# Optimization experiments

Hardware: AMD Instinct MI355X
Metric: run time of the kernel (lower is better)

## Reference

```python
import jax, jax.numpy as jnp
import numpy as np

EPS = 1e-5


def _bn(x, gamma, beta, mean, var):
    # Inference-mode BatchNorm2d over channel dim (NCHW -> axis 1).
    inv = gamma / jnp.sqrt(var + EPS)
    return x * inv[None, :, None, None] + (beta - mean * inv)[None, :, None, None]


def setup_inputs() -> dict:
    key = jax.random.key(0)
    ks = jax.random.split(key, 6)
    N, Cin, Cout, T, V = 64, 64, 128, 300, 25
    x = jax.random.normal(ks[0], (N, Cin, T, V), dtype=jnp.float32)
    A = jax.random.uniform(ks[1], (V, V), dtype=jnp.float32)  # fixed adjacency (non-trainable buffer)
    edge = jnp.ones((V, V), dtype=jnp.float32)                # learnable edge mask, init ones
    gcn_w = jax.random.normal(ks[2], (Cout, Cin), dtype=jnp.float32) * 0.05
    gcn_b = jnp.zeros((Cout,), dtype=jnp.float32)
    res_w = jax.random.normal(ks[3], (Cout, Cin), dtype=jnp.float32) * 0.05
    res_b = jnp.zeros((Cout,), dtype=jnp.float32)
    return {
        'x': x, 'A': A, 'edge': edge,
        'gcn_w': gcn_w, 'gcn_b': gcn_b,
        'bn_gamma': jnp.ones((Cout,), jnp.float32), 'bn_beta': jnp.zeros((Cout,), jnp.float32),
        'bn_mean': jnp.zeros((Cout,), jnp.float32), 'bn_var': jnp.ones((Cout,), jnp.float32),
        'res_w': res_w, 'res_b': res_b,
        'rbn_gamma': jnp.ones((Cout,), jnp.float32), 'rbn_beta': jnp.zeros((Cout,), jnp.float32),
        'rbn_mean': jnp.zeros((Cout,), jnp.float32), 'rbn_var': jnp.ones((Cout,), jnp.float32),
    }


def reference(x, A, edge, gcn_w, gcn_b, bn_gamma, bn_beta, bn_mean, bn_var,
              res_w, res_b, rbn_gamma, rbn_beta, rbn_mean, rbn_var):
    # x: [N, Cin, T, V]
    # residual branch: 1x1 conv + BN (in_channel != out_channel path)
    res = jnp.einsum('oc,nctv->notv', res_w, x) + res_b[None, :, None, None]
    res = _bn(res, rbn_gamma, rbn_beta, rbn_mean, rbn_var)
    # main branch: 1x1 conv -> adjacency einsum -> BN
    y = jnp.einsum('oc,nctv->notv', gcn_w, x) + gcn_b[None, :, None, None]
    y = jnp.einsum('nctv,vw->nctw', y, A * edge)
    y = _bn(y, bn_gamma, bn_beta, bn_mean, bn_var)
    # keep_prob = 1.0 -> Randomized_DropBlock_Ske / DropBlockT_1d are identity
    return jax.nn.relu(y + res)
```

## Files before the change

kernel.cpp:

```cpp
#include <hip/hip_runtime.h>
#include <stdint.h>

#define N_ 64
#define C_ 64
#define O_ 128
#define T_ 300
#define V_ 25
#define TB 4
#define JB (TB * 32)
#define KB 128
#define LDB 136

typedef __attribute__((ext_vector_type(8))) short short8;
typedef __attribute__((ext_vector_type(4))) float floatx4;

__device__ __forceinline__ short f2bf(float f) {
  unsigned u = __float_as_uint(f);
  unsigned r = (u + 0x7FFFu + ((u >> 16) & 1u)) >> 16;
  return (short)(r & 0xFFFFu);
}

__global__ void sgc_prep(const float* __restrict__ A, const float* __restrict__ edge,
                         const float* __restrict__ gcn_w, const float* __restrict__ gcn_b,
                         const float* __restrict__ bn_g, const float* __restrict__ bn_b,
                         const float* __restrict__ bn_m, const float* __restrict__ bn_v,
                         const float* __restrict__ res_w, const float* __restrict__ res_b,
                         const float* __restrict__ rg, const float* __restrict__ rb,
                         const float* __restrict__ rm, const float* __restrict__ rv,
                         short* __restrict__ Wcat, float* __restrict__ M2p,
                         float* __restrict__ Cwp) {
  const int tid = threadIdx.x;
  for (int i = tid; i < 25 * 32; i += 256) {
    const int v = i >> 5, w = i & 31;
    M2p[i] = (w < 25) ? A[v * 25 + w] * edge[v * 25 + w] : 0.f;
  }
  for (int i = tid; i < O_ * 32; i += 256) {
    const int o = i >> 5, w = i & 31;
    const float inv1 = bn_g[o] * rsqrtf(bn_v[o] + 1e-5f);
    const float inv2 = rg[o] * rsqrtf(rv[o] + 1e-5f);
    float S = 0.f;
    if (w < 25) {
      for (int v = 0; v < 25; ++v) S += A[v * 25 + w] * edge[v * 25 + w];
    }
    Cwp[i] = inv1 * gcn_b[o] * S + (bn_b[o] - bn_m[o] * inv1) + inv2 * res_b[o] +
             (rb[o] - rm[o] * inv2);
  }
  for (int i = tid; i < O_ * KB; i += 256) {
    const int o = i >> 7, k = i & 127;
    const float inv1 = bn_g[o] * rsqrtf(bn_v[o] + 1e-5f);
    const float inv2 = rg[o] * rsqrtf(rv[o] + 1e-5f);
    const float val = (k < 64) ? inv2 * res_w[o * 64 + k] : inv1 * gcn_w[o * 64 + (k - 64)];
    Wcat[i] = f2bf(val);
  }
}

__global__ __launch_bounds__(256, 2) void sgc_main(const float* __restrict__ x,
                                                   const short* __restrict__ Wcat,
                                                   const float* __restrict__ M2p,
                                                   const float* __restrict__ Cw,
                                                   float* __restrict__ out) {
  __shared__ short Bs[JB * LDB];
  const int tid = threadIdx.x;
  const int b = blockIdx.x;
  const int n = b / 75;
  const int t0 = (b % 75) * TB;

  {
    const int tl = tid >> 6;
    const int c = tid & 63;
    const float* xrow = x + (((n * C_ + c) * T_) + (t0 + tl)) * V_;
    float xr[25];
#pragma unroll
    for (int v = 0; v < 25; ++v) xr[v] = xrow[v];
#pragma unroll
    for (int v = 0; v < 25; ++v) Bs[(tl * 32 + v) * LDB + c] = f2bf(xr[v]);
#pragma unroll
    for (int v = 25; v < 32; ++v) {
      Bs[(tl * 32 + v) * LDB + c] = 0;
      Bs[(tl * 32 + v) * LDB + 64 + c] = 0;
    }
    float xa[25];
#pragma unroll
    for (int w = 0; w < 25; ++w) xa[w] = 0.f;
    for (int v = 0; v < 25; ++v) {
      const float xv = xr[v];
      const float* m2 = M2p + v * 32;
#pragma unroll
      for (int w = 0; w < 25; ++w) xa[w] = __builtin_fmaf(xv, m2[w], xa[w]);
    }
#pragma unroll
    for (int w = 0; w < 25; ++w) Bs[(tl * 32 + w) * LDB + 64 + c] = f2bf(xa[w]);
  }
  __syncthreads();

  const int lane = tid & 63;
  const int wv = tid >> 6;
  const int l15 = lane & 15;
  const int quad = lane >> 4;
  const int obase = wv * 32;

  short8 af[2][4];
#pragma unroll
  for (int mt = 0; mt < 2; ++mt) {
#pragma unroll
    for (int kq = 0; kq < 4; ++kq) {
      af[mt][kq] =
          *(const short8*)(Wcat + (obase + mt * 16 + l15) * KB + kq * 32 + quad * 8);
    }
  }

  floatx4 acc[2][8];
#pragma unroll
  for (int mt = 0; mt < 2; ++mt)
#pragma unroll
    for (int jt = 0; jt < 8; ++jt) acc[mt][jt] = (floatx4){0.f, 0.f, 0.f, 0.f};

#pragma unroll
  for (int jt = 0; jt < 8; ++jt) {
#pragma unroll
    for (int kq = 0; kq < 4; ++kq) {
      const short8 bf =
          *(const short8*)(&Bs[(jt * 16 + l15) * LDB + kq * 32 + quad * 8]);
      acc[0][jt] = __builtin_amdgcn_mfma_f32_16x16x32_bf16(af[0][kq], bf, acc[0][jt], 0, 0, 0);
      acc[1][jt] = __builtin_amdgcn_mfma_f32_16x16x32_bf16(af[1][kq], bf, acc[1][jt], 0, 0, 0);
    }
  }

#pragma unroll
  for (int mt = 0; mt < 2; ++mt) {
#pragma unroll
    for (int jt = 0; jt < 8; ++jt) {
      const int j = jt * 16 + l15;
      const int w = j & 31;
      if (w < 25) {
        const int tloc = j >> 5;
        const int o0 = obase + mt * 16 + quad * 4;
        float* op = out + (((n * O_ + o0) * T_) + (t0 + tloc)) * V_ + w;
        const float* cwp = Cw + o0 * 32 + w;
#pragma unroll
        for (int r = 0; r < 4; ++r) {
          const float val = acc[mt][jt][r] + cwp[r * 32];
          op[r * (T_ * V_)] = val > 0.f ? val : 0.f;
        }
      }
    }
  }
}

extern "C" void kernel_launch(void* const* d_in, const int* in_sizes, int n_in,
                              void* d_out, int out_size, void* d_ws, size_t ws_size,
                              hipStream_t stream) {
  const float* x = (const float*)d_in[0];
  const float* A = (const float*)d_in[1];
  const float* edge = (const float*)d_in[2];
  const float* gcn_w = (const float*)d_in[3];
  const float* gcn_b = (const float*)d_in[4];
  const float* bn_g = (const float*)d_in[5];
  const float* bn_b = (const float*)d_in[6];
  const float* bn_m = (const float*)d_in[7];
  const float* bn_v = (const float*)d_in[8];
  const float* res_w = (const float*)d_in[9];
  const float* res_b = (const float*)d_in[10];
  const float* rg = (const float*)d_in[11];
  const float* rb = (const float*)d_in[12];
  const float* rm = (const float*)d_in[13];
  const float* rv = (const float*)d_in[14];

  char* ws = (char*)d_ws;
  short* Wcat = (short*)(ws);
  float* M2p = (float*)(ws + 32768);
  float* Cwp = (float*)(ws + 36864);
  float* out = (float*)d_out;

  hipLaunchKernelGGL(sgc_prep, dim3(1), dim3(256), 0, stream, A, edge, gcn_w, gcn_b,
                     bn_g, bn_b, bn_m, bn_v, res_w, res_b, rg, rb, rm, rv, Wcat, M2p, Cwp);
  hipLaunchKernelGGL(sgc_main, dim3(N_ * (T_ / TB)), dim3(256), 0, stream, x, Wcat, M2p,
                     Cwp, out);
}
```

Baseline: 473.5 us.

## Compute x·A with MFMA and vectorize x loads, overlap with residual GEMM

The per-thread scalar FMA loop computing x times the adjacency matrix is replaced by bf16 MFMA ops. The adjacency matrix is prepacked into MFMA A-fragment layout in the prep kernel, and an extra shared-memory transposed copy of x serves as the B operand. x is now loaded with float4 coalesced reads. The main GEMM is split so the residual half (first K=64) runs before a barrier while the xA half is being written, and launch bounds are raised to 3 blocks per CU. This adds shared memory and a second barrier, and rounds xA's inputs to bf16 before the product, which changes precision slightly.

```diff
diff --git a/kernel.cpp b/kernel.cpp
--- a/kernel.cpp
+++ b/kernel.cpp
@@ -7,9 +7,9 @@
 #define T_ 300
 #define V_ 25
 #define TB 4
-#define JB (TB * 32)
 #define KB 128
 #define LDB 136
+#define LDX 136
 
 typedef __attribute__((ext_vector_type(8))) short short8;
 typedef __attribute__((ext_vector_type(4))) float floatx4;
@@ -27,12 +27,13 @@
                          const float* __restrict__ res_w, const float* __restrict__ res_b,
                          const float* __restrict__ rg, const float* __restrict__ rb,
                          const float* __restrict__ rm, const float* __restrict__ rv,
-                         short* __restrict__ Wcat, float* __restrict__ M2p,
+                         short* __restrict__ Wcat, short* __restrict__ M2A,
                          float* __restrict__ Cwp) {
   const int tid = threadIdx.x;
-  for (int i = tid; i < 25 * 32; i += 256) {
-    const int v = i >> 5, w = i & 31;
-    M2p[i] = (w < 25) ? A[v * 25 + w] * edge[v * 25 + w] : 0.f;
+  for (int idx = tid; idx < 2 * 64 * 8; idx += 256) {
+    const int i = idx & 7, lane = (idx >> 3) & 63, mt2 = idx >> 9;
+    const int v = (lane >> 4) * 8 + i, w = mt2 * 16 + (lane & 15);
+    M2A[idx] = (v < 25 && w < 25) ? f2bf(A[v * 25 + w] * edge[v * 25 + w]) : (short)0;
   }
   for (int i = tid; i < O_ * 32; i += 256) {
     const int o = i >> 5, w = i & 31;
@@ -54,44 +55,17 @@
   }
 }
 
-__global__ __launch_bounds__(256, 2) void sgc_main(const float* __restrict__ x,
+__global__ __launch_bounds__(256, 3) void sgc_main(const float* __restrict__ x,
                                                    const short* __restrict__ Wcat,
-                                                   const float* __restrict__ M2p,
+                                                   const short* __restrict__ M2A,
                                                    const float* __restrict__ Cw,
                                                    float* __restrict__ out) {
-  __shared__ short Bs[JB * LDB];
+  __shared__ short Bs[(TB * 32) * LDB];
+  __shared__ short Xs[C_ * LDX];
   const int tid = threadIdx.x;
   const int b = blockIdx.x;
   const int n = b / 75;
   const int t0 = (b % 75) * TB;
-
-  {
-    const int tl = tid >> 6;
-    const int c = tid & 63;
-    const float* xrow = x + (((n * C_ + c) * T_) + (t0 + tl)) * V_;
-    float xr[25];
-#pragma unroll
-    for (int v = 0; v < 25; ++v) xr[v] = xrow[v];
-#pragma unroll
-    for (int v = 0; v < 25; ++v) Bs[(tl * 32 + v) * LDB + c] = f2bf(xr[v]);
-#pragma unroll
-    for (int v = 25; v < 32; ++v) {
-      Bs[(tl * 32 + v) * LDB + c] = 0;
-      Bs[(tl * 32 + v) * LDB + 64 + c] = 0;
-    }
-    float xa[25];
-#pragma unroll
-    for (int w = 0; w < 25; ++w) xa[w] = 0.f;
-    for (int v = 0; v < 25; ++v) {
-      const float xv = xr[v];
-      const float* m2 = M2p + v * 32;
-#pragma unroll
-      for (int w = 0; w < 25; ++w) xa[w] = __builtin_fmaf(xv, m2[w], xa[w]);
-    }
-#pragma unroll
-    for (int w = 0; w < 25; ++w) Bs[(tl * 32 + w) * LDB + 64 + c] = f2bf(xa[w]);
-  }
-  __syncthreads();
 
   const int lane = tid & 63;
   const int wv = tid >> 6;
@@ -101,12 +75,62 @@
 
   short8 af[2][4];
 #pragma unroll
-  for (int mt = 0; mt < 2; ++mt) {
-#pragma unroll
-    for (int kq = 0; kq < 4; ++kq) {
-      af[mt][kq] =
-          *(const short8*)(Wcat + (obase + mt * 16 + l15) * KB + kq * 32 + quad * 8);
-    }
+  for (int mt = 0; mt < 2; ++mt)
+#pragma unroll
+    for (int kq = 0; kq < 4; ++kq)
+      af[mt][kq] = *(const short8*)(Wcat + (obase + mt * 16 + l15) * KB + kq * 32 + quad * 8);
+  short8 am2[2];
+  am2[0] = *(const short8*)(M2A + lane * 8);
+  am2[1] = *(const short8*)(M2A + (64 + lane) * 8);
+
+  {
+    const int c = tid >> 2, q = tid & 3;
+    const floatx4* xp = (const floatx4*)(x + ((n * C_ + c) * T_ + t0) * V_);
+#pragma unroll
+    for (int i = 0; i < 7; ++i) {
+      const int idx = q + 4 * i;
+      if (idx < 25) {
+        const floatx4 f = xp[idx];
+#pragma unroll
+        for (int e = 0; e < 4; ++e) {
+          const int flat = idx * 4 + e;
+          const int tl = flat / 25;
+          const int v = flat - tl * 25;
+          const short bv = f2bf(f[e]);
+          const int j = tl * 32 + v;
+          Xs[c * LDX + j] = bv;
+          Bs[j * LDB + c] = bv;
+        }
+      }
+    }
+#pragma unroll
+    for (int v = 25; v < 32; ++v) Xs[c * LDX + q * 32 + v] = 0;
+  }
+  __syncthreads();
+
+  {
+    floatx4 xacc[2][4];
+#pragma unroll
+    for (int mt2 = 0; mt2 < 2; ++mt2)
+#pragma unroll
+      for (int nt = 0; nt < 4; ++nt) xacc[mt2][nt] = (floatx4){0.f, 0.f, 0.f, 0.f};
+#pragma unroll
+    for (int nt = 0; nt < 4; ++nt) {
+      const short8 bf = *(const short8*)(Xs + (nt * 16 + l15) * LDX + wv * 32 + quad * 8);
+      xacc[0][nt] = __builtin_amdgcn_mfma_f32_16x16x32_bf16(am2[0], bf, xacc[0][nt], 0, 0, 0);
+      xacc[1][nt] = __builtin_amdgcn_mfma_f32_16x16x32_bf16(am2[1], bf, xacc[1][nt], 0, 0, 0);
+    }
+#pragma unroll
+    for (int mt2 = 0; mt2 < 2; ++mt2)
+#pragma unroll
+      for (int nt = 0; nt < 4; ++nt) {
+        const int c = nt * 16 + l15;
+#pragma unroll
+        for (int r = 0; r < 4; ++r) {
+          const int w = mt2 * 16 + quad * 4 + r;
+          if (w < 25) Bs[(wv * 32 + w) * LDB + 64 + c] = f2bf(xacc[mt2][nt][r]);
+        }
+      }
   }
 
   floatx4 acc[2][8];
@@ -114,13 +138,22 @@
   for (int mt = 0; mt < 2; ++mt)
 #pragma unroll
     for (int jt = 0; jt < 8; ++jt) acc[mt][jt] = (floatx4){0.f, 0.f, 0.f, 0.f};
-
 #pragma unroll
   for (int jt = 0; jt < 8; ++jt) {
 #pragma unroll
-    for (int kq = 0; kq < 4; ++kq) {
-      const short8 bf =
-          *(const short8*)(&Bs[(jt * 16 + l15) * LDB + kq * 32 + quad * 8]);
+    for (int kq = 0; kq < 2; ++kq) {
+      const short8 bf = *(const short8*)(&Bs[(jt * 16 + l15) * LDB + kq * 32 + quad * 8]);
+      acc[0][jt] = __builtin_amdgcn_mfma_f32_16x16x32_bf16(af[0][kq], bf, acc[0][jt], 0, 0, 0);
+      acc[1][jt] = __builtin_amdgcn_mfma_f32_16x16x32_bf16(af[1][kq], bf, acc[1][jt], 0, 0, 0);
+    }
+  }
+  __syncthreads();
+
+#pragma unroll
+  for (int jt = 0; jt < 8; ++jt) {
+#pragma unroll
+    for (int kq = 2; kq < 4; ++kq) {
+      const short8 bf = *(const short8*)(&Bs[(jt * 16 + l15) * LDB + kq * 32 + quad * 8]);
       acc[0][jt] = __builtin_amdgcn_mfma_f32_16x16x32_bf16(af[0][kq], bf, acc[0][jt], 0, 0, 0);
       acc[1][jt] = __builtin_amdgcn_mfma_f32_16x16x32_bf16(af[1][kq], bf, acc[1][jt], 0, 0, 0);
     }
@@ -168,12 +201,12 @@
 
   char* ws = (char*)d_ws;
   short* Wcat = (short*)(ws);
-  float* M2p = (float*)(ws + 32768);
-  float* Cwp = (float*)(ws + 36864);
+  short* M2A = (short*)(ws + 32768);
+  float* Cwp = (float*)(ws + 34816);
   float* out = (float*)d_out;
 
   hipLaunchKernelGGL(sgc_prep, dim3(1), dim3(256), 0, stream, A, edge, gcn_w, gcn_b,
-                     bn_g, bn_b, bn_m, bn_v, res_w, res_b, rg, rb, rm, rv, Wcat, M2p, Cwp);
-  hipLaunchKernelGGL(sgc_main, dim3(N_ * (T_ / TB)), dim3(256), 0, stream, x, Wcat, M2p,
+                     bn_g, bn_b, bn_m, bn_v, res_w, res_b, rg, rb, rm, rv, Wcat, M2A, Cwp);
+  hipLaunchKernelGGL(sgc_main, dim3(N_ * (T_ / TB)), dim3(256), 0, stream, x, Wcat, M2A,
                      Cwp, out);
 }
```

Result: slower. 483.8 us (+2.2%).
